# Kernel tuning notes

Hardware: AMD Instinct MI355X
Metric: run time of the kernel (lower is better)

The kernel has to match this reference:

```python
import jax, jax.numpy as jnp
import numpy as np

# --- model hyperparams (match init_kwargs) ---
N_DIM = 200      # n_dim == nfeat == nhidden (Linear(200,200) hardcoded in source)
NHID = 200
NLAYERS = 8
ALPHA = 0.1
LAMDA = 0.5
B, L = 20, 100   # dialogues x uniform dialogue length
N = B * L        # 2000 utterances per modality -> 3N = 6000 graph nodes
A_DIM, V_DIM, L_DIM, NSPK = 300, 342, 1024, 2


def _linear_params(key, fin, fout):
    s = 1.0 / np.sqrt(fin)
    k1, k2 = jax.random.split(key)
    W = jax.random.uniform(k1, (fin, fout), jnp.float32, -s, s)
    b = jax.random.uniform(k2, (fout,), jnp.float32, -s, s)
    return W, b


def setup_inputs() -> dict:
    key = jax.random.key(0)
    ks = jax.random.split(key, 12)
    a = jax.random.normal(ks[0], (N, A_DIM), jnp.float32)
    v = jax.random.normal(ks[1], (N, V_DIM), jnp.float32)
    l = jax.random.normal(ks[2], (N, L_DIM), jnp.float32)
    qmask = jax.random.uniform(ks[3], (L, B, NSPK), dtype=jnp.float32)
    # dense normalized adjacency over the 3N-node multimodal graph
    adj = jax.random.uniform(ks[4], (3 * N, 3 * N), dtype=jnp.float32) / (3.0 * N)
    Wa, ba = _linear_params(ks[5], A_DIM, N_DIM)
    Wv, bv = _linear_params(ks[6], V_DIM, N_DIM)
    Wl, bl = _linear_params(ks[7], L_DIM, N_DIM)
    spk_emb = jax.random.normal(ks[8], (NSPK, N_DIM), jnp.float32)
    W0, b0 = _linear_params(ks[9], N_DIM, NHID)
    s = 1.0 / np.sqrt(NHID)
    # variant=True -> conv weight is [2*nhidden, nhidden]
    convW = jax.random.uniform(ks[10], (NLAYERS, 2 * NHID, NHID), jnp.float32, -s, s)
    return dict(a=a, v=v, l=l, qmask=qmask, adj=adj,
                Wa=Wa, ba=ba, Wv=Wv, bv=bv, Wl=Wl, bl=bl,
                spk_emb=spk_emb, W0=W0, b0=b0, convW=convW, dia_len=L)


def reference(a, v, l, qmask, adj, Wa, ba, Wv, bv, Wl, bl, spk_emb, W0, b0, convW, dia_len):
    # modality projections
    a = a @ Wa + ba                                   # [N, n_dim]
    v = v @ Wv + bv
    l = l @ Wl + bl
    # qmask: [L, B, n_spk] seq-first -> concat per dialogue (uniform lengths)
    qcat = jnp.transpose(qmask[:dia_len], (1, 0, 2)).reshape(-1, qmask.shape[-1])  # [N, n_spk]
    spk_idx = jnp.argmax(qcat, axis=-1)
    l = l + spk_emb[spk_idx]                          # use_speaker, 'l' in modals
    # big multimodal graph: stack modalities along node axis
    x = jnp.concatenate([a, v, l], axis=0)            # [3N, n_dim]
    # GCNII_lyc (eval mode: dropout identity)
    h0 = jax.nn.relu(x @ W0 + b0)                     # [3N, nhidden]
    thetas = jnp.log(LAMDA / jnp.arange(1, NLAYERS + 1, dtype=jnp.float32) + 1.0)

    def layer(h, wt):
        W, theta = wt
        hi = adj @ h                                  # spmm (dense here)
        support = jnp.concatenate([hi, h0], axis=1)   # variant=True
        r = (1.0 - ALPHA) * hi + ALPHA * h0
        h_new = jax.nn.relu(theta * (support @ W) + (1.0 - theta) * r)
        return h_new, None

    h, _ = jax.lax.scan(layer, h0, (convW, thetas))
    feat = jnp.concatenate([x, h], axis=1)            # use_residue -> [3N, n_dim+nhidden]
    n = a.shape[0]
    # split modality chunks back and fuse on feature axis -> [N, 3*(n_dim+nhidden)]
    return jnp.concatenate([feat[:n], feat[n:2 * n], feat[2 * n:3 * n]], axis=-1)
```

## Files before the change

kernel.cpp:

```cpp
#include <hip/hip_runtime.h>
#include <math.h>

typedef unsigned short u16;
typedef unsigned int u32;
typedef __bf16 bf8_t __attribute__((ext_vector_type(8)));
typedef float f4_t __attribute__((ext_vector_type(4)));
typedef u16 us8_t __attribute__((ext_vector_type(8)));
typedef u16 us4_t __attribute__((ext_vector_type(4)));

#define LDC 224
#define NROWS 6016
#define PLANE (NROWS*LDC)

__device__ __forceinline__ float b2f(u16 x){
  union{u32 u; float f;} c; c.u = ((u32)x)<<16; return c.f;
}
__device__ __forceinline__ u16 f2b(float f){
  union{u32 u; float f;} c; c.f = f;
  u32 b = c.u;
  return (u16)((b + 0x7FFFu + ((b>>16)&1u)) >> 16);
}
__device__ __forceinline__ u16 ldcvt(const void* p, size_t i, int f){
  return f ? f2b(((const float*)p)[i]) : ((const u16*)p)[i];
}
__device__ __forceinline__ void gl16(const u16* g, u16* l){
  __builtin_amdgcn_global_load_lds((const __attribute__((address_space(1))) void*)g,
                                   (__attribute__((address_space(3))) void*)l, 16, 0, 0);
}

__device__ __forceinline__ int detect_inline(const u16* adj, int salt){
  int l = threadIdx.x & 63;
  u16 u = adj[2*(((salt & 1023)<<6) + l)];
  int ex = (u >> 7) & 0xFF;
  bool ok = ((u >> 15) == 0) && (ex >= 0x30) && (ex <= 0x72);
  unsigned long long m = __ballot(ok);
  return (__popcll(m) < 32) ? 1 : 0;
}

__global__ void prep_kernel(const void* __restrict__ adj, u16* __restrict__ adj_bf,
                            const void* __restrict__ Wa, const void* __restrict__ Wv,
                            const void* __restrict__ Wl, const void* __restrict__ W0,
                            const void* __restrict__ convW, const void* __restrict__ qmask,
                            const void* __restrict__ a_in, const void* __restrict__ v_in,
                            const void* __restrict__ spkemb_in,
                            const void* __restrict__ ba, const void* __restrict__ bv,
                            const void* __restrict__ bl, const void* __restrict__ b0,
                            u16* __restrict__ WaT, u16* __restrict__ WvT, u16* __restrict__ WlT,
                            u16* __restrict__ W0T, u16* __restrict__ WtT, u16* __restrict__ WbT,
                            int* __restrict__ spk, u16* __restrict__ x_bf,
                            u16* __restrict__ a_p, u16* __restrict__ v_p,
                            u16* __restrict__ spkem, u16* __restrict__ b_all)
{
  const int y = blockIdx.y;
  const int f = detect_inline((const u16*)adj, blockIdx.x + y*896);
  const int e = blockIdx.x*256 + threadIdx.x;

  if (y >= 29){
    if (!adj_bf) return;
    size_t idx = (size_t)(y-29)*229376 + e;
    if (idx >= (size_t)6016*752) return;
    int row = (int)(idx / 752);
    int k8  = (int)(idx - (size_t)row*752) * 8;
    us8_t vv;
    if (row < 6000){
      if (f){
        const float* src = (const float*)adj + (size_t)row*6000;
        if (k8 + 8 <= 6000){
          f4_t x0 = *(const f4_t*)(src + k8);
          f4_t x1 = *(const f4_t*)(src + k8 + 4);
          #pragma unroll
          for (int j=0;j<4;j++){ vv[j] = f2b(x0[j]); vv[4+j] = f2b(x1[j]); }
        } else {
          #pragma unroll
          for (int j=0;j<8;j++){ int k=k8+j; vv[j] = (k<6000) ? f2b(src[k]) : (u16)0; }
        }
      } else {
        const u16* src = (const u16*)adj + (size_t)row*6000;
        if (k8 + 8 <= 6000){
          vv = *(const us8_t*)(src + k8);
        } else {
          #pragma unroll
          for (int j=0;j<8;j++){ int k=k8+j; vv[j] = (k<6000) ? src[k] : (u16)0; }
        }
      }
    } else {
      #pragma unroll
      for (int j=0;j<8;j++) vv[j] = 0;
    }
    *(us8_t*)(adj_bf + (size_t)row*6016 + k8) = vv;
    return;
  }

  if (y < 20){
    const void* src; u16* dst; int K, kpad; size_t soff = 0;
    if (y == 0){ src=Wa; dst=WaT; K=300; kpad=320; }
    else if (y == 1){ src=Wv; dst=WvT; K=342; kpad=384; }
    else if (y == 2){ src=Wl; dst=WlT; K=1024; kpad=1024; }
    else if (y == 3){ src=W0; dst=W0T; K=200; kpad=256; }
    else if (y < 12){ int i=y-4;  src=convW; soff=(size_t)i*80000;          dst=WtT + i*57344; K=200; kpad=256; }
    else            { int i=y-12; src=convW; soff=(size_t)i*80000 + 40000;  dst=WbT + i*57344; K=200; kpad=256; }
    int total = 224*kpad;
    if (e >= total) return;
    int n = e / kpad, k = e - n*kpad;
    u16 val = 0;
    if (k < K && n < 200) val = ldcvt(src, soff + (size_t)k*200 + n, f);
    dst[e] = val;
    return;
  }
  if (y == 20){
    if (e < 2000){
      int b = e/100, t = e - b*100;
      size_t base = ((size_t)t*20 + b)*2;
      bool one;
      if (f) one = ((const float*)qmask)[base+1] > ((const float*)qmask)[base];
      else   one = b2f(((const u16*)qmask)[base+1]) > b2f(((const u16*)qmask)[base]);
      spk[e] = one ? 1 : 0;
    } else if (e < 2400){
      spkem[e-2000] = ldcvt(spkemb_in, e-2000, f);
    } else if (e < 3200){
      int j = e - 2400; int which = j/200, idx = j - which*200;
      const void* src = (which==0)?ba:(which==1)?bv:(which==2)?bl:b0;
      b_all[j] = ldcvt(src, idx, f);
    }
    return;
  }
  if (y == 21){
    if (e < 16*LDC) x_bf[(size_t)6000*LDC + e] = 0;
    return;
  }
  if (y < 25){
    size_t eg = (size_t)(y-22)*229376 + e;
    if (eg >= (size_t)2048*320) return;
    int row = (int)(eg/320), k = (int)(eg - (size_t)row*320);
    a_p[eg] = (row < 2000 && k < 300) ? ldcvt(a_in, (size_t)row*300 + k, f) : (u16)0;
    return;
  }
  {
    size_t eg = (size_t)(y-25)*229376 + e;
    if (eg >= (size_t)2048*384) return;
    int row = (int)(eg/384), k = (int)(eg - (size_t)row*384);
    v_p[eg] = (row < 2000 && k < 342) ? ldcvt(v_in, (size_t)row*342 + k, f) : (u16)0;
  }
}

template<int WR>
__global__ __launch_bounds__(256, 2)
void gemm_kernel(int dynA, const void* __restrict__ dref, const u16* __restrict__ a_sel,
                 const void* __restrict__ A1, int lda1, int kv1, int kg1, int ks1, const u16* __restrict__ B1, int ldb1,
                 int Mv, int Mout, int spp, int emode,
                 const u16* __restrict__ bias, const u16* __restrict__ spk_e, const int* __restrict__ spk_idx,
                 u16* __restrict__ part_base,
                 u16* __restrict__ outN, u16* __restrict__ outT)
{
  __shared__ u16 ldsA[WR*32*64];
  __shared__ u16 ldsB[224*64];
  const int tid = threadIdx.x;
  const int l = tid & 63;
  const int w = tid >> 6;
  const int wrow = w >> 1, wcol = w & 1;
  const int row0 = blockIdx.x * (WR*32);
  const int lq = l >> 4, lr = l & 15;

  const u16* A16 = (const u16*)A1;
  const float* A32 = (const float*)A1;
  int af32 = 0, lda = lda1, kv = kv1, kg = kg1, Mvl = Mv;
  if (dynA){
    int fd = detect_inline((const u16*)dref, blockIdx.x + blockIdx.y*131);
    if (dynA == 1){
      af32 = fd;
    } else {
      if (fd){ A16 = a_sel; lda = 6016; kv = 6016; kg = 6016; Mvl = 6016; }
    }
  }

  f4_t acc[WR][7];
  #pragma unroll
  for (int i=0;i<WR;i++)
    #pragma unroll
    for (int j=0;j<7;j++){ f4_t z = {0.f,0.f,0.f,0.f}; acc[i][j] = z; }

  int sb = blockIdx.y * spp, se = sb + spp;
  if (se > ks1) se = ks1;

  #pragma unroll 1
  for (int s = sb; s < se; ++s){
    int k0 = s << 6;
    __syncthreads();
    bool alignedA = ((lda & 7) == 0) && (row0 + WR*32 <= Mvl);
    bool gldsA = (!af32) && alignedA && (k0 + 64 <= kg);
    if (gldsA){
      const u16* abase = A16 + k0;
      #pragma unroll
      for (int i=0;i<WR;i++){
        int c = (i<<8) + tid;
        int m = c >> 3, k8p = c & 7;
        int k8 = k8p ^ (m & 7);
        gl16(abase + (size_t)(row0+m)*lda + (k8<<3), &ldsA[c<<3]);
      }
    } else if (af32 && alignedA && (k0 + 64 <= kv)){
      const float* ap = A32 + (size_t)row0*lda + k0;
      #pragma unroll
      for (int i=0;i<WR;i++){
        int c = (i<<8) + tid;
        int m = c >> 3, k8 = c & 7;
        f4_t x0 = *(const f4_t*)(ap + (size_t)m*lda + (k8<<3));
        f4_t x1 = *(const f4_t*)(ap + (size_t)m*lda + (k8<<3) + 4);
        us8_t vv;
        #pragma unroll
        for (int j=0;j<4;j++){ vv[j] = f2b(x0[j]); vv[4+j] = f2b(x1[j]); }
        *(us8_t*)(&ldsA[(m<<6) + ((k8 ^ (m&7))<<3)]) = vv;
      }
    } else {
      #pragma unroll
      for (int i=0;i<WR;i++){
        int c = (i<<8) + tid;
        int m = c >> 3, k8 = c & 7;
        int gr = row0 + m; if (gr > Mvl-1) gr = Mvl-1;
        us8_t vv;
        #pragma unroll
        for (int j=0;j<8;j++){
          int kk = k0 + (k8<<3) + j;
          u16 t = 0;
          if (kk < kv){
            if (af32) t = f2b(A32[(size_t)gr*lda + kk]);
            else      t = A16[(size_t)gr*lda + kk];
          }
          vv[j] = t;
        }
        *(us8_t*)(&ldsA[(m<<6) + ((k8 ^ (m&7))<<3)]) = vv;
      }
    }
    {
      const u16* bbase = B1 + k0;
      #pragma unroll
      for (int i=0;i<7;i++){
        int c = (i<<8) + tid;
        int n = c >> 3, k8p = c & 7;
        int k8 = k8p ^ (n & 7);
        gl16(bbase + (size_t)n*ldb1 + (k8<<3), &ldsB[c<<3]);
      }
    }
    __syncthreads();
    #pragma unroll
    for (int h=0; h<2; ++h){
      bf8_t af[WR], bfr[7];
      int kc = lq + (h<<2);
      #pragma unroll
      for (int rt=0;rt<WR;rt++){
        int m = wrow*(16*WR) + rt*16 + lr;
        af[rt] = *(const bf8_t*)(&ldsA[(m<<6) + ((kc ^ (m&7))<<3)]);
      }
      #pragma unroll
      for (int ct=0;ct<7;ct++){
        int n = wcol*112 + ct*16 + lr;
        bfr[ct] = *(const bf8_t*)(&ldsB[(n<<6) + ((kc ^ (n&7))<<3)]);
      }
      #pragma unroll
      for (int rt=0;rt<WR;rt++)
        #pragma unroll
        for (int ct=0;ct<7;ct++)
          acc[rt][ct] = __builtin_amdgcn_mfma_f32_16x16x32_bf16(af[rt], bfr[ct], acc[rt][ct], 0,0,0);
    }
  }

  #pragma unroll
  for (int rt=0;rt<WR;rt++){
    int r_base = row0 + wrow*(16*WR) + rt*16 + lq*4;
    #pragma unroll
    for (int ct=0;ct<7;ct++){
      int c = wcol*112 + ct*16 + lr;
      f4_t a4 = acc[rt][ct];
      if (emode == 0){
        u16* dst = part_base + (size_t)blockIdx.y * PLANE;
        #pragma unroll
        for (int r=0;r<4;r++) dst[(size_t)(r_base+r)*LDC + c] = f2b(a4[r]);
      } else if (emode == 1){
        float bval = (c < 200) ? b2f(bias[c]) : 0.f;
        #pragma unroll
        for (int r=0;r<4;r++){
          int R = r_base + r;
          if (R < Mout){
            float vv = a4[r] + bval;
            if (spk_e && c < 200) vv += b2f(spk_e[spk_idx[R]*200 + c]);
            outN[(size_t)R*LDC + c] = f2b(vv);
          }
        }
      } else {
        float bval = (c < 200) ? b2f(bias[c]) : 0.f;
        us4_t p;
        #pragma unroll
        for (int r=0;r<4;r++){
          int R = r_base + r;
          float vv = a4[r] + bval; if (vv < 0.f) vv = 0.f;
          u16 q = f2b(vv);
          outN[(size_t)R*LDC + c] = q;
          p[r] = q;
        }
        *(us4_t*)(&outT[(size_t)c*NROWS + r_base]) = p;
      }
    }
  }
}

__global__ __launch_bounds__(256, 2)
void layer_kernel(const u16* __restrict__ part, int nsk,
                  const u16* __restrict__ h0_bf,
                  const u16* __restrict__ Bt, const u16* __restrict__ Bb,
                  float theta, u16* __restrict__ outT)
{
  __shared__ u16 ldsHI[32*256];
  __shared__ u16 ldsH0[32*256];
  __shared__ u16 ldsB[224*64];
  const int tid = threadIdx.x;
  const int l = tid & 63;
  const int w = tid >> 6;
  const int wrow = w >> 1, wcol = w & 1;
  const int row0 = blockIdx.x * 32;
  const int lq = l >> 4, lr = l & 15;

  #pragma unroll
  for (int rr=0; rr<4; ++rr){
    int c = rr*256 + tid;
    int m = c >> 5, ch = c & 31;
    us8_t o;
    if (ch < 28){
      float s[8];
      #pragma unroll
      for (int j=0;j<8;j++) s[j] = 0.f;
      size_t base = (size_t)(row0+m)*LDC + (ch<<3);
      for (int p=0;p<nsk;p++){
        us8_t vv = *(const us8_t*)(part + (size_t)p*PLANE + base);
        #pragma unroll
        for (int j=0;j<8;j++) s[j] += b2f(vv[j]);
      }
      #pragma unroll
      for (int j=0;j<8;j++) o[j] = f2b(s[j]);
    } else {
      #pragma unroll
      for (int j=0;j<8;j++) o[j] = 0;
    }
    *(us8_t*)(&ldsHI[(m<<8) + ((ch ^ (m&7))<<3)]) = o;
    int sch = ch ^ (m&7);
    gl16(h0_bf + (size_t)(row0+m)*LDC + (sch<<3), &ldsH0[c<<3]);
  }

  f4_t acc[7];
  #pragma unroll
  for (int j=0;j<7;j++){ f4_t z = {0.f,0.f,0.f,0.f}; acc[j] = z; }

  #pragma unroll 1
  for (int pair = 0; pair < 2; ++pair){
    const u16* Bp = pair ? Bb : Bt;
    const u16* Alds = pair ? &ldsH0[0] : &ldsHI[0];
    #pragma unroll 1
    for (int s = 0; s < 4; ++s){
      __syncthreads();
      const u16* bbase = Bp + (s<<6);
      #pragma unroll
      for (int i=0;i<7;i++){
        int c = (i<<8) + tid;
        int n = c >> 3, k8p = c & 7;
        int k8 = k8p ^ (n & 7);
        gl16(bbase + (size_t)n*256 + (k8<<3), &ldsB[c<<3]);
      }
      __syncthreads();
      #pragma unroll
      for (int h=0; h<2; ++h){
        int kc = lq + (h<<2);
        int m = wrow*16 + lr;
        bf8_t af = *(const bf8_t*)(&Alds[(m<<8) + (((s<<3) | (kc ^ (m&7)))<<3)]);
        bf8_t bfr[7];
        #pragma unroll
        for (int ct=0;ct<7;ct++){
          int n = wcol*112 + ct*16 + lr;
          bfr[ct] = *(const bf8_t*)(&ldsB[(n<<6) + ((kc ^ (n&7))<<3)]);
        }
        #pragma unroll
        for (int ct=0;ct<7;ct++)
          acc[ct] = __builtin_amdgcn_mfma_f32_16x16x32_bf16(af, bfr[ct], acc[ct], 0,0,0);
      }
    }
  }

  int r_base = row0 + wrow*16 + lq*4;
  #pragma unroll
  for (int ct=0;ct<7;ct++){
    int c = wcol*112 + ct*16 + lr;
    int cc8 = c >> 3, ce = c & 7;
    us4_t p;
    #pragma unroll
    for (int r=0;r<4;r++){
      int mr = wrow*16 + lq*4 + r;
      int ix = (mr<<8) + ((cc8 ^ (mr&7))<<3) + ce;
      float rrv = 0.9f*b2f(ldsHI[ix]) + 0.1f*b2f(ldsH0[ix]);
      float vv = theta*acc[ct][r] + (1.f - theta)*rrv;
      if (vv < 0.f) vv = 0.f;
      p[r] = f2b(vv);
    }
    *(us4_t*)(&outT[(size_t)c*NROWS + r_base]) = p;
  }
}

__device__ __forceinline__ u16 sent(u16 t, u16 snan, u16 sbig){
  u16 mag = t & 0x7FFF;
  if (mag >= 0x7F80) return snan;
  if (mag >= 0x4480) return sbig;
  return t;
}
__global__ void out_kernel(const void* __restrict__ adjv,
                           const u16* __restrict__ x_bf, const u16* __restrict__ hT,
                           void* __restrict__ outp)
{
  __shared__ u16 tile[64*216];
  const int of32 = detect_inline((const u16*)adjv, blockIdx.x + blockIdx.y*37);
  u16* o16 = (u16*)outp;
  float* o32 = (float*)outp;
  const int tid = threadIdx.x;
  const int n0 = blockIdx.x*64;
  const int m = blockIdx.y;
  for (int cc = tid; cc < 1600; cc += 256){
    int r = cc/25, c8 = cc - r*25;
    int n = n0 + r;
    int rr = n < 2000 ? n : 1999;
    us8_t vv = *(const us8_t*)(x_bf + ((size_t)(m*2000 + rr))*LDC + c8*8);
    #pragma unroll
    for (int j=0;j<8;j++) vv[j] = sent(vv[j], 0x46EA, 0x46DB);
    if (n < 2000){
      size_t off = (size_t)n*1200 + m*400 + c8*8;
      if (!of32) *(us8_t*)(o16 + off) = vv;
      else {
        f4_t lo, hi;
        #pragma unroll
        for (int j=0;j<4;j++){ lo[j] = b2f(vv[j]); hi[j] = b2f(vv[4+j]); }
        *(f4_t*)(o32 + off) = lo; *(f4_t*)(o32 + off + 4) = hi;
      }
    }
  }
  for (int cc = tid; cc < 1600; cc += 256){
    int c = cc >> 3, ng = cc & 7;
    int nb = n0 + ng*8;
    if (nb > 1992) nb = 1992;
    us8_t vv = *(const us8_t*)(hT + (size_t)c*NROWS + m*2000 + nb);
    #pragma unroll
    for (int j=0;j<8;j++) tile[(ng*8+j)*216 + c] = sent(vv[j], 0x469C, 0x468C);
  }
  __syncthreads();
  for (int cc = tid; cc < 1600; cc += 256){
    int r = cc/25, c8 = cc - r*25;
    int n = n0 + r;
    if (n < 2000){
      us8_t vv = *(const us8_t*)(&tile[r*216 + c8*8]);
      size_t off = (size_t)n*1200 + m*400 + 200 + c8*8;
      if (!of32) *(us8_t*)(o16 + off) = vv;
      else {
        f4_t lo, hi;
        #pragma unroll
        for (int j=0;j<4;j++){ lo[j] = b2f(vv[j]); hi[j] = b2f(vv[4+j]); }
        *(f4_t*)(o32 + off) = lo; *(f4_t*)(o32 + off + 4) = hi;
      }
    }
  }
}

extern "C" void kernel_launch(void* const* d_in, const int* in_sizes, int n_in,
                              void* d_out, int out_size, void* d_ws, size_t ws_size,
                              hipStream_t stream)
{
  const void* a     = d_in[0];
  const void* v     = d_in[1];
  const void* l     = d_in[2];
  const void* qmask = d_in[3];
  const void* adj   = d_in[4];
  const void* Wa    = d_in[5];
  const void* ba    = d_in[6];
  const void* Wv    = d_in[7];
  const void* bv    = d_in[8];
  const void* Wl    = d_in[9];
  const void* bl    = d_in[10];
  const void* spk_emb = d_in[11];
  const void* W0    = d_in[12];
  const void* b0    = d_in[13];
  const void* convW = d_in[14];

  int cfg = (ws_size >= (size_t)125*1024*1024) ? 2
          : (ws_size >= (size_t)48*1024*1024) ? 1 : 0;
  const int SK = (cfg >= 1) ? 8 : 2;
  const int SPP = (94 + SK - 1) / SK;

  char* ws = (char*)d_ws;
  size_t off = 0;
  auto alloc = [&](size_t bytes)->char*{
    char* p = ws + off; off = (off + bytes + 255) & ~(size_t)255; return p;
  };
  u16*  x_bf  = (u16*) alloc((size_t)PLANE*2);
  u16*  h0_bf = (u16*) alloc((size_t)PLANE*2);
  u16*  hT    = (u16*) alloc((size_t)PLANE*2);
  u16*  a_p   = (u16*) alloc((size_t)2048*320*2);
  u16*  v_p   = (u16*) alloc((size_t)2048*384*2);
  u16* WaT = (u16*)alloc(224*320*2);
  u16* WvT = (u16*)alloc(224*384*2);
  u16* WlT = (u16*)alloc(224*1024*2);
  u16* W0T = (u16*)alloc(224*256*2);
  u16* WtT = (u16*)alloc((size_t)8*224*256*2);
  u16* WbT = (u16*)alloc((size_t)8*224*256*2);
  int* spk = (int*)alloc(2000*4);
  u16* spkem = (u16*)alloc(400*2);
  u16* b_all = (u16*)alloc(800*2);
  u16* part = (u16*)alloc((size_t)SK*PLANE*2);
  u16* adj_bf = (cfg == 2) ? (u16*)alloc((size_t)6016*6016*2) : nullptr;

  prep_kernel<<<dim3(896, (cfg==2) ? 49 : 29),256,0,stream>>>(adj, adj_bf,
      Wa,Wv,Wl,W0,convW,qmask, a,v,spk_emb, ba,bv,bl,b0,
      WaT,WvT,WlT,W0T,WtT,WbT, spk, x_bf, a_p,v_p, spkem, b_all);

  gemm_kernel<1><<<dim3(64,1),256,0,stream>>>(0, nullptr, nullptr,
      a_p,320,320,320,5, WaT,320,
      2048,2000, 5, 1, b_all, nullptr, nullptr,
      nullptr, x_bf, nullptr);
  gemm_kernel<1><<<dim3(64,1),256,0,stream>>>(0, nullptr, nullptr,
      v_p,384,384,384,6, WvT,384,
      2048,2000, 6, 1, b_all+200, nullptr, nullptr,
      nullptr, x_bf + (size_t)2000*LDC, nullptr);
  gemm_kernel<1><<<dim3(64,1),256,0,stream>>>(1, adj, nullptr,
      l,1024,1024,1024,16, WlT,1024,
      2000,2000, 16, 1, b_all+400, spkem, spk,
      nullptr, x_bf + (size_t)4000*LDC, nullptr);

  gemm_kernel<1><<<dim3(188,1),256,0,stream>>>(0, nullptr, nullptr,
      x_bf,LDC,LDC,256,4, W0T,256,
      NROWS,NROWS, 4, 2, b_all+600, nullptr, nullptr,
      nullptr, h0_bf, hT);

  for (int i=0;i<8;i++){
    float theta = logf(0.5f/(float)(i+1) + 1.0f);
    if (cfg == 2)
      gemm_kernel<2><<<dim3(94,SK),256,0,stream>>>(3, adj, adj_bf,
          adj,6000,6000,6000,94, hT,NROWS,
          6000,0, SPP, 0, nullptr, nullptr, nullptr,
          part, nullptr, nullptr);
    else
      gemm_kernel<2><<<dim3(94,SK),256,0,stream>>>(1, adj, nullptr,
          adj,6000,6000,6000,94, hT,NROWS,
          6000,0, SPP, 0, nullptr, nullptr, nullptr,
          part, nullptr, nullptr);
    layer_kernel<<<dim3(188),256,0,stream>>>(part, SK, h0_bf,
        WtT + (size_t)i*57344, WbT + (size_t)i*57344, theta, hT);
  }

  out_kernel<<<dim3(32,3),256,0,stream>>>(adj, x_bf, hT, (void*)d_out);
}
```

Measured before the change: 686.7 us.

## Double-buffer LDS tiles in GEMM kernels and tune split-K and prep grid

Adds a two-stage LDS ping-pong to the main GEMM and the conv-layer kernel, prefetching the next K-tile with async global-to-LDS loads while the current tile is computed. Explicit vmcnt waits and raw barriers stand in for the full syncthreads pairs. Split-K for the adjacency GEMM drops from 8 to 5, and the adjacency conversion now handles two chunks per thread on a smaller grid. The extra LDS may lower occupancy, and the hand-written vmcnt counts depend on how the compiler emits the loads.

```diff
diff --git a/kernel.cpp b/kernel.cpp
--- a/kernel.cpp
+++ b/kernel.cpp
@@ -57,37 +57,42 @@
 
   if (y >= 29){
     if (!adj_bf) return;
-    size_t idx = (size_t)(y-29)*229376 + e;
-    if (idx >= (size_t)6016*752) return;
-    int row = (int)(idx / 752);
-    int k8  = (int)(idx - (size_t)row*752) * 8;
-    us8_t vv;
-    if (row < 6000){
-      if (f){
-        const float* src = (const float*)adj + (size_t)row*6000;
-        if (k8 + 8 <= 6000){
-          f4_t x0 = *(const f4_t*)(src + k8);
-          f4_t x1 = *(const f4_t*)(src + k8 + 4);
-          #pragma unroll
-          for (int j=0;j<4;j++){ vv[j] = f2b(x0[j]); vv[4+j] = f2b(x1[j]); }
+    size_t ch0 = ((size_t)(y-29)*229376 + e)*2;
+    #pragma unroll
+    for (int q=0; q<2; ++q){
+      size_t idx = ch0 + q;
+      if (idx < (size_t)6016*752){
+        int row = (int)(idx / 752);
+        int k8  = (int)(idx - (size_t)row*752) * 8;
+        us8_t vv;
+        if (row < 6000){
+          if (f){
+            const float* src = (const float*)adj + (size_t)row*6000;
+            if (k8 + 8 <= 6000){
+              f4_t x0 = *(const f4_t*)(src + k8);
+              f4_t x1 = *(const f4_t*)(src + k8 + 4);
+              #pragma unroll
+              for (int j=0;j<4;j++){ vv[j] = f2b(x0[j]); vv[4+j] = f2b(x1[j]); }
+            } else {
+              #pragma unroll
+              for (int j=0;j<8;j++){ int k=k8+j; vv[j] = (k<6000) ? f2b(src[k]) : (u16)0; }
+            }
+          } else {
+            const u16* src = (const u16*)adj + (size_t)row*6000;
+            if (k8 + 8 <= 6000){
+              vv = *(const us8_t*)(src + k8);
+            } else {
+              #pragma unroll
+              for (int j=0;j<8;j++){ int k=k8+j; vv[j] = (k<6000) ? src[k] : (u16)0; }
+            }
+          }
         } else {
           #pragma unroll
-          for (int j=0;j<8;j++){ int k=k8+j; vv[j] = (k<6000) ? f2b(src[k]) : (u16)0; }
+          for (int j=0;j<8;j++) vv[j] = 0;
         }
-      } else {
-        const u16* src = (const u16*)adj + (size_t)row*6000;
-        if (k8 + 8 <= 6000){
-          vv = *(const us8_t*)(src + k8);
-        } else {
-          #pragma unroll
-          for (int j=0;j<8;j++){ int k=k8+j; vv[j] = (k<6000) ? src[k] : (u16)0; }
-        }
-      }
-    } else {
-      #pragma unroll
-      for (int j=0;j<8;j++) vv[j] = 0;
-    }
-    *(us8_t*)(adj_bf + (size_t)row*6016 + k8) = vv;
+        *(us8_t*)(adj_bf + (size_t)row*6016 + k8) = vv;
+      }
+    }
     return;
   }
 
@@ -152,8 +157,8 @@
                  u16* __restrict__ part_base,
                  u16* __restrict__ outN, u16* __restrict__ outT)
 {
-  __shared__ u16 ldsA[WR*32*64];
-  __shared__ u16 ldsB[224*64];
+  __shared__ u16 ldsA[2][WR*32*64];
+  __shared__ u16 ldsB[2][224*64];
   const int tid = threadIdx.x;
   const int l = tid & 63;
   const int w = tid >> 6;
@@ -182,65 +187,27 @@
   int sb = blockIdx.y * spp, se = sb + spp;
   if (se > ks1) se = ks1;
 
-  #pragma unroll 1
-  for (int s = sb; s < se; ++s){
-    int k0 = s << 6;
-    __syncthreads();
-    bool alignedA = ((lda & 7) == 0) && (row0 + WR*32 <= Mvl);
-    bool gldsA = (!af32) && alignedA && (k0 + 64 <= kg);
-    if (gldsA){
-      const u16* abase = A16 + k0;
-      #pragma unroll
-      for (int i=0;i<WR;i++){
-        int c = (i<<8) + tid;
-        int m = c >> 3, k8p = c & 7;
-        int k8 = k8p ^ (m & 7);
-        gl16(abase + (size_t)(row0+m)*lda + (k8<<3), &ldsA[c<<3]);
-      }
-    } else if (af32 && alignedA && (k0 + 64 <= kv)){
-      const float* ap = A32 + (size_t)row0*lda + k0;
-      #pragma unroll
-      for (int i=0;i<WR;i++){
-        int c = (i<<8) + tid;
-        int m = c >> 3, k8 = c & 7;
-        f4_t x0 = *(const f4_t*)(ap + (size_t)m*lda + (k8<<3));
-        f4_t x1 = *(const f4_t*)(ap + (size_t)m*lda + (k8<<3) + 4);
-        us8_t vv;
-        #pragma unroll
-        for (int j=0;j<4;j++){ vv[j] = f2b(x0[j]); vv[4+j] = f2b(x1[j]); }
-        *(us8_t*)(&ldsA[(m<<6) + ((k8 ^ (m&7))<<3)]) = vv;
-      }
-    } else {
-      #pragma unroll
-      for (int i=0;i<WR;i++){
-        int c = (i<<8) + tid;
-        int m = c >> 3, k8 = c & 7;
-        int gr = row0 + m; if (gr > Mvl-1) gr = Mvl-1;
-        us8_t vv;
-        #pragma unroll
-        for (int j=0;j<8;j++){
-          int kk = k0 + (k8<<3) + j;
-          u16 t = 0;
-          if (kk < kv){
-            if (af32) t = f2b(A32[(size_t)gr*lda + kk]);
-            else      t = A16[(size_t)gr*lda + kk];
-          }
-          vv[j] = t;
-        }
-        *(us8_t*)(&ldsA[(m<<6) + ((k8 ^ (m&7))<<3)]) = vv;
-      }
-    }
-    {
-      const u16* bbase = B1 + k0;
-      #pragma unroll
-      for (int i=0;i<7;i++){
-        int c = (i<<8) + tid;
-        int n = c >> 3, k8p = c & 7;
-        int k8 = k8p ^ (n & 7);
-        gl16(bbase + (size_t)n*ldb1 + (k8<<3), &ldsB[c<<3]);
-      }
-    }
-    __syncthreads();
+  auto stageA = [&](int p, int k0){
+    const u16* abase = A16 + k0;
+    #pragma unroll
+    for (int i=0;i<WR;i++){
+      int c = (i<<8) + tid;
+      int m = c >> 3, k8p = c & 7;
+      int k8 = k8p ^ (m & 7);
+      gl16(abase + (size_t)(row0+m)*lda + (k8<<3), &ldsA[p][c<<3]);
+    }
+  };
+  auto stageB = [&](int p, int k0){
+    const u16* bbase = B1 + k0;
+    #pragma unroll
+    for (int i=0;i<7;i++){
+      int c = (i<<8) + tid;
+      int n = c >> 3, k8p = c & 7;
+      int k8 = k8p ^ (n & 7);
+      gl16(bbase + (size_t)n*ldb1 + (k8<<3), &ldsB[p][c<<3]);
+    }
+  };
+  auto computeT = [&](int p){
     #pragma unroll
     for (int h=0; h<2; ++h){
       bf8_t af[WR], bfr[7];
@@ -248,18 +215,86 @@
       #pragma unroll
       for (int rt=0;rt<WR;rt++){
         int m = wrow*(16*WR) + rt*16 + lr;
-        af[rt] = *(const bf8_t*)(&ldsA[(m<<6) + ((kc ^ (m&7))<<3)]);
+        af[rt] = *(const bf8_t*)(&ldsA[p][(m<<6) + ((kc ^ (m&7))<<3)]);
       }
       #pragma unroll
       for (int ct=0;ct<7;ct++){
         int n = wcol*112 + ct*16 + lr;
-        bfr[ct] = *(const bf8_t*)(&ldsB[(n<<6) + ((kc ^ (n&7))<<3)]);
+        bfr[ct] = *(const bf8_t*)(&ldsB[p][(n<<6) + ((kc ^ (n&7))<<3)]);
       }
       #pragma unroll
       for (int rt=0;rt<WR;rt++)
         #pragma unroll
         for (int ct=0;ct<7;ct++)
           acc[rt][ct] = __builtin_amdgcn_mfma_f32_16x16x32_bf16(af[rt], bfr[ct], acc[rt][ct], 0,0,0);
+    }
+  };
+
+  bool pipe = (!af32) && ((lda & 7) == 0) && (row0 + WR*32 <= Mvl)
+              && (se > sb) && (se*64 <= kg);
+
+  if (pipe){
+    stageA(0, sb<<6); stageB(0, sb<<6);
+    int p = 0;
+    #pragma unroll 1
+    for (int s = sb; s < se; ++s){
+      if (s + 1 < se){
+        stageA(p^1, (s+1)<<6); stageB(p^1, (s+1)<<6);
+        if (WR == 2) asm volatile("s_waitcnt vmcnt(9)" ::: "memory");
+        else         asm volatile("s_waitcnt vmcnt(8)" ::: "memory");
+      } else {
+        asm volatile("s_waitcnt vmcnt(0)" ::: "memory");
+      }
+      __builtin_amdgcn_s_barrier();
+      computeT(p);
+      __builtin_amdgcn_s_barrier();
+      p ^= 1;
+    }
+  } else {
+    #pragma unroll 1
+    for (int s = sb; s < se; ++s){
+      int k0 = s << 6;
+      __syncthreads();
+      bool alignedA = ((lda & 7) == 0) && (row0 + WR*32 <= Mvl);
+      bool gldsA = (!af32) && alignedA && (k0 + 64 <= kg);
+      if (gldsA){
+        stageA(0, k0);
+      } else if (af32 && alignedA && (k0 + 64 <= kv)){
+        const float* ap = A32 + (size_t)row0*lda + k0;
+        #pragma unroll
+        for (int i=0;i<WR;i++){
+          int c = (i<<8) + tid;
+          int m = c >> 3, k8 = c & 7;
+          f4_t x0 = *(const f4_t*)(ap + (size_t)m*lda + (k8<<3));
+          f4_t x1 = *(const f4_t*)(ap + (size_t)m*lda + (k8<<3) + 4);
+          us8_t vv;
+          #pragma unroll
+          for (int j=0;j<4;j++){ vv[j] = f2b(x0[j]); vv[4+j] = f2b(x1[j]); }
+          *(us8_t*)(&ldsA[0][(m<<6) + ((k8 ^ (m&7))<<3)]) = vv;
+        }
+      } else {
+        #pragma unroll
+        for (int i=0;i<WR;i++){
+          int c = (i<<8) + tid;
+          int m = c >> 3, k8 = c & 7;
+          int gr = row0 + m; if (gr > Mvl-1) gr = Mvl-1;
+          us8_t vv;
+          #pragma unroll
+          for (int j=0;j<8;j++){
+            int kk = k0 + (k8<<3) + j;
+            u16 t = 0;
+            if (kk < kv){
+              if (af32) t = f2b(A32[(size_t)gr*lda + kk]);
+              else      t = A16[(size_t)gr*lda + kk];
+            }
+            vv[j] = t;
+          }
+          *(us8_t*)(&ldsA[0][(m<<6) + ((k8 ^ (m&7))<<3)]) = vv;
+        }
+      }
+      stageB(0, k0);
+      __syncthreads();
+      computeT(0);
     }
   }
 
@@ -287,16 +322,16 @@
         }
       } else {
         float bval = (c < 200) ? b2f(bias[c]) : 0.f;
-        us4_t p;
+        us4_t p4;
         #pragma unroll
         for (int r=0;r<4;r++){
           int R = r_base + r;
           float vv = a4[r] + bval; if (vv < 0.f) vv = 0.f;
           u16 q = f2b(vv);
           outN[(size_t)R*LDC + c] = q;
-          p[r] = q;
+          p4[r] = q;
         }
-        *(us4_t*)(&outT[(size_t)c*NROWS + r_base]) = p;
+        *(us4_t*)(&outT[(size_t)c*NROWS + r_base]) = p4;
       }
     }
   }
@@ -310,7 +345,7 @@
 {
   __shared__ u16 ldsHI[32*256];
   __shared__ u16 ldsH0[32*256];
-  __shared__ u16 ldsB[224*64];
+  __shared__ u16 ldsB[2][224*64];
   const int tid = threadIdx.x;
   const int l = tid & 63;
   const int w = tid >> 6;
@@ -344,42 +379,53 @@
     gl16(h0_bf + (size_t)(row0+m)*LDC + (sch<<3), &ldsH0[c<<3]);
   }
 
+  auto stageB = [&](int p, int t){
+    const u16* Bp = (t>>2) ? Bb : Bt;
+    const u16* bbase = Bp + ((t&3)<<6);
+    #pragma unroll
+    for (int i=0;i<7;i++){
+      int c = (i<<8) + tid;
+      int n = c >> 3, k8p = c & 7;
+      int k8 = k8p ^ (n & 7);
+      gl16(bbase + (size_t)n*256 + (k8<<3), &ldsB[p][c<<3]);
+    }
+  };
+
   f4_t acc[7];
   #pragma unroll
   for (int j=0;j<7;j++){ f4_t z = {0.f,0.f,0.f,0.f}; acc[j] = z; }
 
+  stageB(0, 0);
+  __syncthreads();
+  int p = 0;
   #pragma unroll 1
-  for (int pair = 0; pair < 2; ++pair){
-    const u16* Bp = pair ? Bb : Bt;
-    const u16* Alds = pair ? &ldsH0[0] : &ldsHI[0];
-    #pragma unroll 1
-    for (int s = 0; s < 4; ++s){
-      __syncthreads();
-      const u16* bbase = Bp + (s<<6);
-      #pragma unroll
-      for (int i=0;i<7;i++){
-        int c = (i<<8) + tid;
-        int n = c >> 3, k8p = c & 7;
-        int k8 = k8p ^ (n & 7);
-        gl16(bbase + (size_t)n*256 + (k8<<3), &ldsB[c<<3]);
-      }
-      __syncthreads();
-      #pragma unroll
-      for (int h=0; h<2; ++h){
-        int kc = lq + (h<<2);
-        int m = wrow*16 + lr;
-        bf8_t af = *(const bf8_t*)(&Alds[(m<<8) + (((s<<3) | (kc ^ (m&7)))<<3)]);
-        bf8_t bfr[7];
-        #pragma unroll
-        for (int ct=0;ct<7;ct++){
-          int n = wcol*112 + ct*16 + lr;
-          bfr[ct] = *(const bf8_t*)(&ldsB[(n<<6) + ((kc ^ (n&7))<<3)]);
-        }
-        #pragma unroll
-        for (int ct=0;ct<7;ct++)
-          acc[ct] = __builtin_amdgcn_mfma_f32_16x16x32_bf16(af, bfr[ct], acc[ct], 0,0,0);
-      }
-    }
+  for (int t = 0; t < 8; ++t){
+    if (t < 7){
+      stageB(p^1, t+1);
+      asm volatile("s_waitcnt vmcnt(7)" ::: "memory");
+    } else {
+      asm volatile("s_waitcnt vmcnt(0)" ::: "memory");
+    }
+    __builtin_amdgcn_s_barrier();
+    const u16* Alds = (t>>2) ? &ldsH0[0] : &ldsHI[0];
+    int sloc = t & 3;
+    #pragma unroll
+    for (int h=0; h<2; ++h){
+      int kc = lq + (h<<2);
+      int m = wrow*16 + lr;
+      bf8_t af = *(const bf8_t*)(&Alds[(m<<8) + (((sloc<<3) | (kc ^ (m&7)))<<3)]);
+      bf8_t bfr[7];
+      #pragma unroll
+      for (int ct=0;ct<7;ct++){
+        int n = wcol*112 + ct*16 + lr;
+        bfr[ct] = *(const bf8_t*)(&ldsB[p][(n<<6) + ((kc ^ (n&7))<<3)]);
+      }
+      #pragma unroll
+      for (int ct=0;ct<7;ct++)
+        acc[ct] = __builtin_amdgcn_mfma_f32_16x16x32_bf16(af, bfr[ct], acc[ct], 0,0,0);
+    }
+    __builtin_amdgcn_s_barrier();
+    p ^= 1;
   }
 
   int r_base = row0 + wrow*16 + lq*4;
@@ -387,7 +433,7 @@
   for (int ct=0;ct<7;ct++){
     int c = wcol*112 + ct*16 + lr;
     int cc8 = c >> 3, ce = c & 7;
-    us4_t p;
+    us4_t p4;
     #pragma unroll
     for (int r=0;r<4;r++){
       int mr = wrow*16 + lq*4 + r;
@@ -395,9 +441,9 @@
       float rrv = 0.9f*b2f(ldsHI[ix]) + 0.1f*b2f(ldsH0[ix]);
       float vv = theta*acc[ct][r] + (1.f - theta)*rrv;
       if (vv < 0.f) vv = 0.f;
-      p[r] = f2b(vv);
-    }
-    *(us4_t*)(&outT[(size_t)c*NROWS + r_base]) = p;
+      p4[r] = f2b(vv);
+    }
+    *(us4_t*)(&outT[(size_t)c*NROWS + r_base]) = p4;
   }
 }
 
@@ -484,7 +530,7 @@
 
   int cfg = (ws_size >= (size_t)125*1024*1024) ? 2
           : (ws_size >= (size_t)48*1024*1024) ? 1 : 0;
-  const int SK = (cfg >= 1) ? 8 : 2;
+  const int SK = (cfg >= 1) ? 5 : 2;
   const int SPP = (94 + SK - 1) / SK;
 
   char* ws = (char*)d_ws;
@@ -509,7 +555,7 @@
   u16* part = (u16*)alloc((size_t)SK*PLANE*2);
   u16* adj_bf = (cfg == 2) ? (u16*)alloc((size_t)6016*6016*2) : nullptr;
 
-  prep_kernel<<<dim3(896, (cfg==2) ? 49 : 29),256,0,stream>>>(adj, adj_bf,
+  prep_kernel<<<dim3(896, (cfg==2) ? 39 : 29),256,0,stream>>>(adj, adj_bf,
       Wa,Wv,Wl,W0,convW,qmask, a,v,spk_emb, ba,bv,bl,b0,
       WaT,WvT,WlT,W0T,WtT,WbT, spk, x_bf, a_p,v_p, spkem, b_all);
 
```

New measurement: 682.9 us. About the same (-0.6%).
